# Kernel optimization log

Measured on AMD Instinct MI355X. Metric: run time of the kernel, lower is better.

Reference implementation:

```python
import jax, jax.numpy as jnp
import numpy as np

N_NODES = 100000
N_EDGES = 1600000
N_KEEP = 1280000  # int(N_EDGES * (1 - thr_a)), thr_a = 0.2
F_IN = 128
F_OUT = 128


def setup_inputs() -> dict:
    key = jax.random.key(0)
    ks = jax.random.split(key, 7)
    x = jax.random.normal(ks[0], (N_NODES, F_IN), dtype=jnp.float32)
    W = jax.random.normal(ks[1], (F_OUT, F_IN), dtype=jnp.float32) * (1.0 / np.sqrt(F_IN))
    bias = jax.random.normal(ks[2], (F_OUT,), dtype=jnp.float32)
    edge_src = jax.random.randint(ks[3], (N_EDGES,), 0, N_NODES, dtype=jnp.int32)
    edge_dst = jax.random.randint(ks[4], (N_EDGES,), 0, N_NODES, dtype=jnp.int32)
    edge_weight = jax.random.uniform(ks[5], (N_EDGES,), dtype=jnp.float32)
    idx_keep = jax.random.randint(ks[6], (N_KEEP,), 0, N_EDGES, dtype=jnp.int32)
    return {"x": x, "W": W, "bias": bias, "edge_src": edge_src,
            "edge_dst": edge_dst, "edge_weight": edge_weight, "idx_keep": idx_keep}


def reference(x, W, bias, edge_src, edge_dst, edge_weight, idx_keep):
    # Linear transform (pyg GCNConv lin has bias=False): h = x @ W.T  -> [N, F_out]
    h = jnp.einsum('nf,of->no', x, W)
    # Edge pruning: keep a random subset of edges (scheme_a='keep')
    src = edge_src[idx_keep]          # [M_keep]
    dst = edge_dst[idx_keep]          # [M_keep]
    ew = edge_weight[idx_keep]        # [M_keep]
    # propagate: message_j = h[src] * ew ; scatter-add into dst
    msg = h[src] * ew[:, None]        # [M_keep, F_out]
    out = jax.ops.segment_sum(msg, dst, num_segments=N_NODES)
    # GCNConv separate bias
    out = out + bias
    return out
```

## Files before the change

### kernel.cpp

```cpp
#include <hip/hip_runtime.h>

#define F 128
#define LDS_STRIDE 136
#define BUCKET 48

typedef __attribute__((ext_vector_type(8))) short short8;
typedef __attribute__((ext_vector_type(8))) unsigned short u16x8;
typedef __attribute__((ext_vector_type(4))) float floatx4;

__device__ __forceinline__ unsigned short f32_to_bf16(float x) {
    unsigned u = __float_as_uint(x);
    unsigned r = u + 0x7FFFu + ((u >> 16) & 1u);
    return (unsigned short)(r >> 16);
}
__device__ __forceinline__ float bf16_to_f32(unsigned short h) {
    return __uint_as_float(((unsigned)h) << 16);
}

__global__ __launch_bounds__(256, 2) void gemm_mfma(const float4* __restrict__ x4,
                                                    const float4* __restrict__ W4,
                                                    unsigned short* __restrict__ h2,
                                                    int n_nodes) {
    __shared__ short xs[128 * LDS_STRIDE];
    __shared__ short wls[128 * LDS_STRIDE];
    const int tid = threadIdx.x;
    const int node0 = blockIdx.x * 128;

    for (int i = tid; i < 128 * 32; i += 256) {
        int row = i >> 5, c4 = i & 31;
        float4 v = W4[i];
        ushort4 b;
        b.x = f32_to_bf16(v.x); b.y = f32_to_bf16(v.y);
        b.z = f32_to_bf16(v.z); b.w = f32_to_bf16(v.w);
        *(ushort4*)&wls[row * LDS_STRIDE + c4 * 4] = b;
    }
    for (int i = tid; i < 128 * 32; i += 256) {
        int row = i >> 5, c4 = i & 31;
        int n = node0 + row;
        float4 v = (n < n_nodes) ? x4[(size_t)n * 32 + c4] : make_float4(0.f, 0.f, 0.f, 0.f);
        ushort4 b;
        b.x = f32_to_bf16(v.x); b.y = f32_to_bf16(v.y);
        b.z = f32_to_bf16(v.z); b.w = f32_to_bf16(v.w);
        *(ushort4*)&xs[row * LDS_STRIDE + c4 * 4] = b;
    }
    __syncthreads();

    const int wave = tid >> 6, lane = tid & 63;
    const int row16 = lane & 15, quad = lane >> 4;
    const int wrow0 = wave * 32;

    floatx4 acc[2][8];
    #pragma unroll
    for (int r = 0; r < 2; ++r)
        #pragma unroll
        for (int c = 0; c < 8; ++c)
            acc[r][c] = (floatx4){0.f, 0.f, 0.f, 0.f};

    #pragma unroll
    for (int s = 0; s < 4; ++s) {
        const int koff = s * 32 + quad * 8;
        short8 a[2];
        #pragma unroll
        for (int r = 0; r < 2; ++r)
            a[r] = *(const short8*)&xs[(wrow0 + r * 16 + row16) * LDS_STRIDE + koff];
        #pragma unroll
        for (int c = 0; c < 8; ++c) {
            short8 b = *(const short8*)&wls[(c * 16 + row16) * LDS_STRIDE + koff];
            acc[0][c] = __builtin_amdgcn_mfma_f32_16x16x32_bf16(a[0], b, acc[0][c], 0, 0, 0);
            acc[1][c] = __builtin_amdgcn_mfma_f32_16x16x32_bf16(a[1], b, acc[1][c], 0, 0, 0);
        }
    }

    #pragma unroll
    for (int r = 0; r < 2; ++r) {
        #pragma unroll
        for (int reg = 0; reg < 4; ++reg) {
            int n = node0 + wrow0 + r * 16 + quad * 4 + reg;
            if (n < n_nodes) {
                #pragma unroll
                for (int c = 0; c < 8; ++c)
                    h2[(size_t)n * F + c * 16 + row16] = f32_to_bf16(acc[r][c][reg]);
            }
        }
    }
}

__global__ __launch_bounds__(256) void fill_direct(const int* __restrict__ idx_keep,
                                                   const int* __restrict__ edge_dst,
                                                   int* __restrict__ cnt,
                                                   int* __restrict__ perm, int m) {
    int e = blockIdx.x * 256 + threadIdx.x;
    if (e < m) {
        int ke = idx_keep[e];
        int d = edge_dst[ke];
        int p = atomicAdd(&cnt[d], 1);
        if (p < BUCKET) perm[d * BUCKET + p] = ke;
    }
}

__global__ __launch_bounds__(256) void pull_nodes4(const u16x8* __restrict__ h8,
                                                   const int* __restrict__ edge_src,
                                                   const float* __restrict__ edge_weight,
                                                   const int* __restrict__ cnt,
                                                   const int* __restrict__ perm,
                                                   const float4* __restrict__ bias4,
                                                   float4* __restrict__ out4,
                                                   int n_nodes) {
    const int node = blockIdx.x * 4 + (threadIdx.x >> 6);
    const int lane = threadIdx.x & 63;
    if (node >= n_nodes) return;

    const int deg = min(cnt[node], BUCKET);
    const int eh = lane >> 4, fl = lane & 15;
    float acc[8];
    #pragma unroll
    for (int i = 0; i < 8; ++i) acc[i] = 0.0f;

    int s = 0; float w = 0.0f;
    if (lane < deg) {
        int ke = perm[node * BUCKET + lane];
        s = edge_src[ke];
        w = edge_weight[ke];
    }
    for (int j = 0; j < deg; j += 4) {
        int jj = j + eh;
        int take = (jj < deg) ? jj : j;
        int   sj = __shfl(s, take, 64);
        float wj = __shfl(w, take, 64);
        if (jj >= deg) wj = 0.0f;
        u16x8 hv = h8[(size_t)sj * 16 + fl];
        #pragma unroll
        for (int i = 0; i < 8; ++i)
            acc[i] += bf16_to_f32((unsigned short)hv[i]) * wj;
    }
    #pragma unroll
    for (int i = 0; i < 8; ++i) {
        acc[i] += __shfl_xor(acc[i], 16, 64);
        acc[i] += __shfl_xor(acc[i], 32, 64);
    }
    if (lane < 16) {
        float4 b0 = bias4[fl * 2], b1 = bias4[fl * 2 + 1];
        out4[(size_t)node * 32 + fl * 2]     = make_float4(acc[0] + b0.x, acc[1] + b0.y, acc[2] + b0.z, acc[3] + b0.w);
        out4[(size_t)node * 32 + fl * 2 + 1] = make_float4(acc[4] + b1.x, acc[5] + b1.y, acc[6] + b1.z, acc[7] + b1.w);
    }
}

extern "C" void kernel_launch(void* const* d_in, const int* in_sizes, int n_in,
                              void* d_out, int out_size, void* d_ws, size_t ws_size,
                              hipStream_t stream) {
    const float* x           = (const float*)d_in[0];
    const float* W           = (const float*)d_in[1];
    const float* bias        = (const float*)d_in[2];
    const int*   edge_src    = (const int*)d_in[3];
    const int*   edge_dst    = (const int*)d_in[4];
    const float* edge_weight = (const float*)d_in[5];
    const int*   idx_keep    = (const int*)d_in[6];
    float* out = (float*)d_out;

    const int n_nodes = in_sizes[0] / F;
    const int m_keep  = in_sizes[6];

    char* ws = (char*)d_ws;
    unsigned short* h2 = (unsigned short*)ws;
    size_t p = (size_t)n_nodes * F * 2;
    int* cnt = (int*)(ws + p);   p += (size_t)n_nodes * 4;
    int* perm = (int*)(ws + p);

    hipMemsetAsync(cnt, 0, (size_t)n_nodes * 4, stream);

    gemm_mfma<<<(n_nodes + 127) / 128, 256, 0, stream>>>(
        (const float4*)x, (const float4*)W, h2, n_nodes);

    fill_direct<<<(m_keep + 255) / 256, 256, 0, stream>>>(
        idx_keep, edge_dst, cnt, perm, m_keep);

    pull_nodes4<<<(n_nodes + 3) / 4, 256, 0, stream>>>(
        (const u16x8*)h2, edge_src, edge_weight, cnt, perm,
        (const float4*)bias, (float4*)out, n_nodes);
}
```

Before: 286.6 us.

## Fold count reset into GEMM, add nontemporal loads/stores, two edges per thread

Zeroes the per-node counter array inside the GEMM kernel instead of issuing a separate memset, which removes one launch. Adds nontemporal hints to streaming loads of x, idx_keep and perm, and to the stores of perm and the output, so this data is kept from polluting cache. The fill kernel now handles two edges per thread with half the blocks. Nontemporal stores to perm may make its later reads in the pull kernel miss cache.

```diff
diff --git a/kernel.cpp b/kernel.cpp
--- a/kernel.cpp
+++ b/kernel.cpp
@@ -7,6 +7,7 @@
 typedef __attribute__((ext_vector_type(8))) short short8;
 typedef __attribute__((ext_vector_type(8))) unsigned short u16x8;
 typedef __attribute__((ext_vector_type(4))) float floatx4;
+typedef __attribute__((ext_vector_type(4))) float f32x4;
 
 __device__ __forceinline__ unsigned short f32_to_bf16(float x) {
     unsigned u = __float_as_uint(x);
@@ -20,11 +21,15 @@
 __global__ __launch_bounds__(256, 2) void gemm_mfma(const float4* __restrict__ x4,
                                                     const float4* __restrict__ W4,
                                                     unsigned short* __restrict__ h2,
+                                                    int* __restrict__ cnt,
                                                     int n_nodes) {
     __shared__ short xs[128 * LDS_STRIDE];
     __shared__ short wls[128 * LDS_STRIDE];
     const int tid = threadIdx.x;
     const int node0 = blockIdx.x * 128;
+
+    for (int i = blockIdx.x * 256 + tid; i < n_nodes; i += gridDim.x * 256)
+        cnt[i] = 0;
 
     for (int i = tid; i < 128 * 32; i += 256) {
         int row = i >> 5, c4 = i & 31;
@@ -37,10 +42,12 @@
     for (int i = tid; i < 128 * 32; i += 256) {
         int row = i >> 5, c4 = i & 31;
         int n = node0 + row;
-        float4 v = (n < n_nodes) ? x4[(size_t)n * 32 + c4] : make_float4(0.f, 0.f, 0.f, 0.f);
+        f32x4 v = (n < n_nodes)
+                      ? __builtin_nontemporal_load((const f32x4*)&x4[(size_t)n * 32 + c4])
+                      : (f32x4){0.f, 0.f, 0.f, 0.f};
         ushort4 b;
-        b.x = f32_to_bf16(v.x); b.y = f32_to_bf16(v.y);
-        b.z = f32_to_bf16(v.z); b.w = f32_to_bf16(v.w);
+        b.x = f32_to_bf16(v[0]); b.y = f32_to_bf16(v[1]);
+        b.z = f32_to_bf16(v[2]); b.w = f32_to_bf16(v[3]);
         *(ushort4*)&xs[row * LDS_STRIDE + c4 * 4] = b;
     }
     __syncthreads();
@@ -89,12 +96,17 @@
                                                    const int* __restrict__ edge_dst,
                                                    int* __restrict__ cnt,
                                                    int* __restrict__ perm, int m) {
-    int e = blockIdx.x * 256 + threadIdx.x;
-    if (e < m) {
-        int ke = idx_keep[e];
-        int d = edge_dst[ke];
-        int p = atomicAdd(&cnt[d], 1);
-        if (p < BUCKET) perm[d * BUCKET + p] = ke;
+    const int base = blockIdx.x * 512 + threadIdx.x;
+    #pragma unroll
+    for (int k = 0; k < 2; ++k) {
+        int e = base + k * 256;
+        if (e < m) {
+            int ke = __builtin_nontemporal_load(&idx_keep[e]);
+            int d = edge_dst[ke];
+            int p = atomicAdd(&cnt[d], 1);
+            if (p < BUCKET)
+                __builtin_nontemporal_store(ke, &perm[d * BUCKET + p]);
+        }
     }
 }
 
@@ -118,7 +130,7 @@
 
     int s = 0; float w = 0.0f;
     if (lane < deg) {
-        int ke = perm[node * BUCKET + lane];
+        int ke = __builtin_nontemporal_load(&perm[node * BUCKET + lane]);
         s = edge_src[ke];
         w = edge_weight[ke];
     }
@@ -140,8 +152,10 @@
     }
     if (lane < 16) {
         float4 b0 = bias4[fl * 2], b1 = bias4[fl * 2 + 1];
-        out4[(size_t)node * 32 + fl * 2]     = make_float4(acc[0] + b0.x, acc[1] + b0.y, acc[2] + b0.z, acc[3] + b0.w);
-        out4[(size_t)node * 32 + fl * 2 + 1] = make_float4(acc[4] + b1.x, acc[5] + b1.y, acc[6] + b1.z, acc[7] + b1.w);
+        f32x4 o0 = {acc[0] + b0.x, acc[1] + b0.y, acc[2] + b0.z, acc[3] + b0.w};
+        f32x4 o1 = {acc[4] + b1.x, acc[5] + b1.y, acc[6] + b1.z, acc[7] + b1.w};
+        __builtin_nontemporal_store(o0, (f32x4*)&out4[(size_t)node * 32 + fl * 2]);
+        __builtin_nontemporal_store(o1, (f32x4*)&out4[(size_t)node * 32 + fl * 2 + 1]);
     }
 }
 
@@ -166,12 +180,11 @@
     int* cnt = (int*)(ws + p);   p += (size_t)n_nodes * 4;
     int* perm = (int*)(ws + p);
 
-    hipMemsetAsync(cnt, 0, (size_t)n_nodes * 4, stream);
 
     gemm_mfma<<<(n_nodes + 127) / 128, 256, 0, stream>>>(
-        (const float4*)x, (const float4*)W, h2, n_nodes);
+        (const float4*)x, (const float4*)W, h2, cnt, n_nodes);
 
-    fill_direct<<<(m_keep + 255) / 256, 256, 0, stream>>>(
+    fill_direct<<<(m_keep + 511) / 512, 256, 0, stream>>>(
         idx_keep, edge_dst, cnt, perm, m_keep);
 
     pull_nodes4<<<(n_nodes + 3) / 4, 256, 0, stream>>>(
```

Result: no change. 284.9 us (-0.6%).
